# Kernel tuning notes

Hardware: AMD Instinct MI355X
Metric: run time of the kernel (lower is better)

Reference implementation:

```python
import jax, jax.numpy as jnp
import numpy as np

D_MODEL = 1024
N_HEADS = 16
D_K = D_MODEL // N_HEADS


def setup_inputs() -> dict:
    key = jax.random.key(0)
    ks = jax.random.split(key, 9)
    s = 1.0 / np.sqrt(D_MODEL)
    inp = {
        "x": jax.random.normal(ks[0], (4, 2048, D_MODEL), dtype=jnp.float32),
        "wq": jax.random.normal(ks[1], (D_MODEL, D_MODEL), dtype=jnp.float32) * s,
        "bq": jax.random.normal(ks[2], (D_MODEL,), dtype=jnp.float32) * 0.01,
        "wk": jax.random.normal(ks[3], (D_MODEL, D_MODEL), dtype=jnp.float32) * s,
        "bk": jax.random.normal(ks[4], (D_MODEL,), dtype=jnp.float32) * 0.01,
        "wv": jax.random.normal(ks[5], (D_MODEL, D_MODEL), dtype=jnp.float32) * s,
        "bv": jax.random.normal(ks[6], (D_MODEL,), dtype=jnp.float32) * 0.01,
        "wo": jax.random.normal(ks[7], (D_MODEL, D_MODEL), dtype=jnp.float32) * s,
        "bo": jax.random.normal(ks[8], (D_MODEL,), dtype=jnp.float32) * 0.01,
    }
    return inp


def reference(x, wq, bq, wk, bk, wv, bv, wo, bo):
    B, S, _ = x.shape
    # QKV projections (weights stored [in, out] so y = x @ w + b)
    q = (x @ wq + bq).reshape(B, S, N_HEADS, D_K).transpose(0, 2, 1, 3)  # [B,H,S,Dk]
    k = (x @ wk + bk).reshape(B, S, N_HEADS, D_K).transpose(0, 2, 1, 3)
    v = (x @ wv + bv).reshape(B, S, N_HEADS, D_K).transpose(0, 2, 1, 3)
    scale = 1.0 / jnp.sqrt(jnp.asarray(D_K, dtype=x.dtype))
    scores = jnp.einsum("bhqd,bhkd->bhqk", q, k) * scale  # [B,H,S,S]
    attn = jax.nn.softmax(scores, axis=-1)
    out = jnp.einsum("bhqk,bhkd->bhqd", attn, v)  # [B,H,S,Dk]
    out = out.transpose(0, 2, 1, 3).reshape(B, S, D_MODEL)
    return out @ wo + bo
```

## Files before the change

### kernel.cpp

```cpp
#include <hip/hip_runtime.h>

#define D_MODEL 1024
#define NH 16
#define DK 64
#define BB 4
#define SS 2048
#define MROWS (BB*SS)

typedef __attribute__((ext_vector_type(4))) float f32x4;
typedef __attribute__((ext_vector_type(16))) float f32x16;
typedef __attribute__((ext_vector_type(8))) short short8;
typedef __attribute__((ext_vector_type(4))) float float4v;
typedef __attribute__((ext_vector_type(2))) unsigned u32x2;

typedef const __attribute__((address_space(1))) void* gas_t;
typedef __attribute__((address_space(3))) void* las_t;

static __device__ __forceinline__ ushort f2bf(float f) {
  union { float f; unsigned u; } v; v.f = f;
  unsigned r = 0x7fffu + ((v.u >> 16) & 1u);
  return (ushort)((v.u + r) >> 16);
}

#define VM_WAIT(N)                                              \
  do {                                                          \
    asm volatile("s_waitcnt vmcnt(" #N ")" ::: "memory");       \
    __builtin_amdgcn_sched_barrier(0);                          \
  } while (0)

#define LGKM0()                                                 \
  do {                                                          \
    asm volatile("s_waitcnt lgkmcnt(0)" ::: "memory");          \
    __builtin_amdgcn_sched_barrier(0);                          \
  } while (0)

__global__ __launch_bounds__(256) void convert_x_k(const float* __restrict__ x,
                                                   ushort* __restrict__ xb) {
  int i = blockIdx.x * 256 + threadIdx.x;
  float4v v = ((const float4v*)x)[i];
  ushort4 o;
  o.x = f2bf(v.x); o.y = f2bf(v.y); o.z = f2bf(v.z); o.w = f2bf(v.w);
  ((ushort4*)xb)[i] = o;
}

__global__ __launch_bounds__(256) void convert_wt4_k(const float* __restrict__ w0,
                                                     const float* __restrict__ w1,
                                                     const float* __restrict__ w2,
                                                     const float* __restrict__ w3,
                                                     ushort* __restrict__ t0,
                                                     ushort* __restrict__ t1,
                                                     ushort* __restrict__ t2,
                                                     ushort* __restrict__ t3) {
  __shared__ float tile[64][65];
  const float* w; ushort* wt;
  switch (blockIdx.z) {
    case 0: w = w0; wt = t0; break;
    case 1: w = w1; wt = t1; break;
    case 2: w = w2; wt = t2; break;
    default: w = w3; wt = t3; break;
  }
  int bx = blockIdx.x, by = blockIdx.y;
  int tx = threadIdx.x & 63, ty = threadIdx.x >> 6;
#pragma unroll
  for (int i = 0; i < 16; ++i) {
    int r = i * 4 + ty;
    tile[r][tx] = w[(size_t)(by * 64 + r) * D_MODEL + bx * 64 + tx];
  }
  __syncthreads();
#pragma unroll
  for (int i = 0; i < 16; ++i) {
    int r = i * 4 + ty;
    wt[(size_t)(bx * 64 + r) * D_MODEL + by * 64 + tx] = f2bf(tile[tx][r]);
  }
}

__global__ __launch_bounds__(512) void gemm_qkv_k(const ushort* __restrict__ A,
                                                  const ushort* __restrict__ Bt,
                                                  const float* __restrict__ bq,
                                                  const float* __restrict__ bk,
                                                  const float* __restrict__ bv,
                                                  ushort* __restrict__ Qw,
                                                  ushort* __restrict__ Kw,
                                                  ushort* __restrict__ Vw,
                                                  float qscale) {
  const int K = D_MODEL;
  __shared__ __align__(16) ushort As[3][256 * 64];
  __shared__ __align__(16) ushort Bs[3][128 * 64];
  const int nbn = 24;
  int bid = blockIdx.x;
  int wg = (bid & 7) * 96 + (bid >> 3);
  int bm = wg / nbn, bn = wg % nbn;
  const int t = threadIdx.x;
  const int l = t & 63;
  const int w = t >> 6;
  const int g = l >> 4, q = l & 15;
  const int wr = w >> 1, wc = w & 1;
  const int qs = q & 7;

  f32x4 acc[4][4];
#pragma unroll
  for (int m = 0; m < 4; ++m)
#pragma unroll
    for (int n = 0; n < 4; ++n) acc[m][n] = f32x4{0.f, 0.f, 0.f, 0.f};

  const ushort* Ab = A + (size_t)bm * 256 * K;
  const ushort* Bb = Bt + (size_t)bn * 128 * K;

#define GSTAGE(BUF, KT)                                                                       \
  do {                                                                                        \
    _Pragma("unroll") for (int i_ = 0; i_ < 4; ++i_) {                                        \
      int c_ = i_ * 512 + t;                                                                  \
      int r_ = c_ >> 3;                                                                       \
      int gc_ = (c_ & 7) ^ (r_ & 7);                                                          \
      __builtin_amdgcn_global_load_lds((gas_t)(Ab + (size_t)r_ * K + (KT) * 64 + gc_ * 8),    \
                                       (las_t)(&As[BUF][c_ * 8]), 16, 0, 0);                  \
    }                                                                                         \
    _Pragma("unroll") for (int i_ = 0; i_ < 2; ++i_) {                                        \
      int c_ = i_ * 512 + t;                                                                  \
      int r_ = c_ >> 3;                                                                       \
      int gc_ = (c_ & 7) ^ (r_ & 7);                                                          \
      __builtin_amdgcn_global_load_lds((gas_t)(Bb + (size_t)r_ * K + (KT) * 64 + gc_ * 8),    \
                                       (las_t)(&Bs[BUF][c_ * 8]), 16, 0, 0);                  \
    }                                                                                         \
  } while (0)

  GSTAGE(0, 0);
  GSTAGE(1, 1);

  for (int kt = 0; kt < 16; ++kt) {
    if (kt + 2 < 16) {
      GSTAGE((kt + 2) % 3, kt + 2);
      VM_WAIT(12);
    } else if (kt + 1 < 16) {
      VM_WAIT(6);
    } else {
      VM_WAIT(0);
    }
    __builtin_amdgcn_s_barrier();
    __builtin_amdgcn_sched_barrier(0);

    const ushort* Ac = As[kt % 3];
    const ushort* Bc = Bs[kt % 3];

    short8 bf[4][2];
#pragma unroll
    for (int n = 0; n < 4; ++n)
#pragma unroll
      for (int ks = 0; ks < 2; ++ks)
        bf[n][ks] = *(const short8*)(Bc + (wc * 64 + n * 16 + q) * 64 + (((ks * 4 + g) ^ qs) * 8));

#pragma unroll
    for (int mh = 0; mh < 2; ++mh) {
      short8 af[2][2];
#pragma unroll
      for (int m2 = 0; m2 < 2; ++m2)
#pragma unroll
        for (int ks = 0; ks < 2; ++ks)
          af[m2][ks] = *(const short8*)(Ac + (wr * 64 + (mh * 2 + m2) * 16 + q) * 64 + (((ks * 4 + g) ^ qs) * 8));
      LGKM0();
      __builtin_amdgcn_s_setprio(1);
#pragma unroll
      for (int m2 = 0; m2 < 2; ++m2)
#pragma unroll
        for (int n = 0; n < 4; ++n)
#pragma unroll
          for (int ks = 0; ks < 2; ++ks)
            acc[mh * 2 + m2][n] =
                __builtin_amdgcn_mfma_f32_16x16x32_bf16(af[m2][ks], bf[n][ks], acc[mh * 2 + m2][n], 0, 0, 0);
      __builtin_amdgcn_s_setprio(0);
    }

    __builtin_amdgcn_sched_barrier(0);
    __builtin_amdgcn_s_barrier();
  }
#undef GSTAGE

  const int sec = (bn * 128) >> 10;
  const float* bias = sec == 0 ? bq : (sec == 1 ? bk : bv);
  const float scale = sec == 0 ? qscale : 1.0f;
  ushort* dst = sec == 0 ? Qw : Kw;
  const int rbase0 = bm * 256 + wr * 64 + g * 4;
  const int cbase = (bn * 128 + wc * 64 + q) & 1023;
#pragma unroll
  for (int m = 0; m < 4; ++m) {
    int r0 = rbase0 + m * 16;
#pragma unroll
    for (int n = 0; n < 4; ++n) {
      int c = cbase + n * 16;
      float bv_ = bias[c];
      if (sec == 2) {
        ushort4 pk;
        pk.x = f2bf(acc[m][n][0] + bv_);
        pk.y = f2bf(acc[m][n][1] + bv_);
        pk.z = f2bf(acc[m][n][2] + bv_);
        pk.w = f2bf(acc[m][n][3] + bv_);
        size_t off = (((size_t)((r0 >> 11) * NH + (c >> 6))) * DK + (c & 63)) * (size_t)SS + (r0 & (SS - 1));
        *(ushort4*)(Vw + off) = pk;
      } else {
#pragma unroll
        for (int j = 0; j < 4; ++j) {
          int r = r0 + j;
          float v = (acc[m][n][j] + bv_) * scale;
          size_t off = (((size_t)((r >> 11) * NH + (c >> 6))) * SS + (r & (SS - 1))) * DK + (c & 63);
          dst[off] = f2bf(v);
        }
      }
    }
  }
}

__global__ __launch_bounds__(256) void gemm_out_k(const ushort* __restrict__ A,
                                                  const ushort* __restrict__ Bt,
                                                  const float* __restrict__ bias,
                                                  float* __restrict__ outp) {
  const int K = D_MODEL;
  __shared__ __align__(16) ushort As[2][128 * 32];
  __shared__ __align__(16) ushort Bs[2][128 * 32];
  const int nbn = 8;
  int bid = blockIdx.x;
  int wg = (bid & 7) * 64 + (bid >> 3);
  int bm = wg / nbn, bn = wg % nbn;
  const int t = threadIdx.x;
  const int l = t & 63;
  const int w = t >> 6;
  const int g = l >> 4, q = l & 15;
  const int wr = w >> 1, wc = w & 1;

  f32x4 acc[4][4];
#pragma unroll
  for (int m = 0; m < 4; ++m)
#pragma unroll
    for (int n = 0; n < 4; ++n) acc[m][n] = f32x4{0.f, 0.f, 0.f, 0.f};

  const ushort* Ab = A + (size_t)bm * 128 * K;
  const ushort* Bb = Bt + (size_t)bn * 128 * K;

#define GSTAGE(BUF, KT)                                                                      \
  do {                                                                                       \
    _Pragma("unroll") for (int i_ = 0; i_ < 2; ++i_) {                                       \
      int c_ = i_ * 256 + t;                                                                 \
      __builtin_amdgcn_global_load_lds((gas_t)(Ab + (size_t)(c_ >> 2) * K + (KT) + (c_ & 3) * 8), \
                                       (las_t)(As[BUF] + c_ * 8), 16, 0, 0);                 \
      __builtin_amdgcn_global_load_lds((gas_t)(Bb + (size_t)(c_ >> 2) * K + (KT) + (c_ & 3) * 8), \
                                       (las_t)(Bs[BUF] + c_ * 8), 16, 0, 0);                 \
    }                                                                                        \
  } while (0)

  GSTAGE(0, 0);
  int cur = 0;

  for (int kt = 0; kt < K; kt += 32) {
    if (kt + 32 < K) {
      GSTAGE(cur ^ 1, kt + 32);
      VM_WAIT(4);
    } else {
      VM_WAIT(0);
    }
    __builtin_amdgcn_s_barrier();
    __builtin_amdgcn_sched_barrier(0);
    short8 af[4], bf[4];
#pragma unroll
    for (int m = 0; m < 4; ++m)
      af[m] = *(const short8*)(As[cur] + (wr * 64 + m * 16 + q) * 32 + g * 8);
#pragma unroll
    for (int n = 0; n < 4; ++n)
      bf[n] = *(const short8*)(Bs[cur] + (wc * 64 + n * 16 + q) * 32 + g * 8);
#pragma unroll
    for (int m = 0; m < 4; ++m)
#pragma unroll
      for (int n = 0; n < 4; ++n)
        acc[m][n] = __builtin_amdgcn_mfma_f32_16x16x32_bf16(af[m], bf[n], acc[m][n], 0, 0, 0);
    __builtin_amdgcn_sched_barrier(0);
    __builtin_amdgcn_s_barrier();
    cur ^= 1;
  }
#undef GSTAGE

  const int rbase0 = bm * 128 + wr * 64 + g * 4;
  const int cbase = bn * 128 + wc * 64 + q;
#pragma unroll
  for (int m = 0; m < 4; ++m) {
    int r0 = rbase0 + m * 16;
#pragma unroll
    for (int n = 0; n < 4; ++n) {
      int c = cbase + n * 16;
      float bv = bias[c];
#pragma unroll
      for (int j = 0; j < 4; ++j)
        outp[(size_t)(r0 + j) * D_MODEL + c] = acc[m][n][j] + bv;
    }
  }
}

__global__ __launch_bounds__(256, 4) void attn_k(const ushort* __restrict__ Qm,
                                                 const ushort* __restrict__ Km,
                                                 const ushort* __restrict__ Vm,
                                                 ushort* __restrict__ Ob) {
  __shared__ __align__(16) ushort Ks[2][64 * 64];
  __shared__ __align__(16) ushort Vs[2][64 * 64];
  const int bid = blockIdx.x;
  const int logical = (bid & 7) * 128 + (bid >> 3);
  const int bh = logical >> 4;
  const int qblk = logical & 15;
  const int t = threadIdx.x, l = t & 63, w = t >> 6;
  const int q = l & 31, h = l >> 5;
  const int qsw = q & 7;

  const ushort* Qb = Qm + ((size_t)bh * SS + qblk * 128 + w * 32) * DK;
  const ushort* Kb = Km + (size_t)bh * SS * DK;
  const ushort* Vb = Vm + (size_t)bh * DK * SS;

  short8 qf[4];
#pragma unroll
  for (int ks = 0; ks < 4; ++ks)
    qf[ks] = *(const short8*)(Qb + q * DK + ks * 16 + h * 8);

  f32x16 oacc[2];
#pragma unroll
  for (int d = 0; d < 2; ++d)
#pragma unroll
    for (int r = 0; r < 16; ++r) oacc[d][r] = 0.f;
  float lrun = 0.f;

  const int cg = (l & 7) ^ ((l >> 3) & 7);

#define STAGE(B, KT)                                                                        \
  do {                                                                                      \
    _Pragma("unroll") for (int i_ = 0; i_ < 2; ++i_) {                                      \
      int row_ = w * 16 + i_ * 8 + (l >> 3);                                                \
      __builtin_amdgcn_global_load_lds((gas_t)(Kb + (size_t)((KT) + row_) * DK + cg * 8),   \
                                       (las_t)(Ks[B] + (w * 16 + i_ * 8) * 64 + l * 8),     \
                                       16, 0, 0);                                           \
      __builtin_amdgcn_global_load_lds((gas_t)(Vb + (size_t)row_ * SS + (KT) + cg * 8),     \
                                       (las_t)(Vs[B] + (w * 16 + i_ * 8) * 64 + l * 8),     \
                                       16, 0, 0);                                           \
    }                                                                                       \
  } while (0)

  STAGE(0, 0);
  int cur = 0;

  for (int kt = 0; kt < SS; kt += 64) {
    __syncthreads();
    if (kt + 64 < SS) STAGE(cur ^ 1, kt + 64);

    const ushort* Kc = Ks[cur];
    const ushort* Vc = Vs[cur];

    f32x16 sc[2];
#pragma unroll
    for (int n = 0; n < 2; ++n)
#pragma unroll
      for (int r = 0; r < 16; ++r) sc[n][r] = 0.f;

    __builtin_amdgcn_s_setprio(1);
#pragma unroll
    for (int ks = 0; ks < 4; ++ks) {
      int ch = ((ks * 2 + h) ^ qsw) * 8;
      short8 kf0 = *(const short8*)(Kc + q * 64 + ch);
      short8 kf1 = *(const short8*)(Kc + (32 + q) * 64 + ch);
      sc[0] = __builtin_amdgcn_mfma_f32_32x32x16_bf16(kf0, qf[ks], sc[0], 0, 0, 0);
      sc[1] = __builtin_amdgcn_mfma_f32_32x32x16_bf16(kf1, qf[ks], sc[1], 0, 0, 0);
    }
    __builtin_amdgcn_s_setprio(0);

#pragma unroll
    for (int n = 0; n < 2; ++n)
#pragma unroll
      for (int r = 0; r < 16; ++r) sc[n][r] = __builtin_amdgcn_exp2f(sc[n][r]);

    float s8[8];
#pragma unroll
    for (int i = 0; i < 8; ++i)
      s8[i] = (sc[0][i] + sc[0][i + 8]) + (sc[1][i] + sc[1][i + 8]);
#pragma unroll
    for (int i = 0; i < 4; ++i) s8[i] += s8[i + 4];
    lrun += (s8[0] + s8[1]) + (s8[2] + s8[3]);

    short8 pf[4];
#pragma unroll
    for (int n = 0; n < 2; ++n) {
      unsigned wv[8];
#pragma unroll
      for (int Qd = 0; Qd < 4; ++Qd) {
        unsigned w0, w1;
        asm("v_cvt_pk_bf16_f32 %0, %1, %2" : "=v"(w0) : "v"(sc[n][Qd * 4 + 0]), "v"(sc[n][Qd * 4 + 1]));
        asm("v_cvt_pk_bf16_f32 %0, %1, %2" : "=v"(w1) : "v"(sc[n][Qd * 4 + 2]), "v"(sc[n][Qd * 4 + 3]));
        wv[Qd * 2] = w0; wv[Qd * 2 + 1] = w1;
      }
#pragma unroll
      for (int m = 0; m < 2; ++m) {
        u32x2 r0 = __builtin_amdgcn_permlane32_swap(wv[(2 * m) * 2 + 0], wv[(2 * m + 1) * 2 + 0], false, false);
        u32x2 r1 = __builtin_amdgcn_permlane32_swap(wv[(2 * m) * 2 + 1], wv[(2 * m + 1) * 2 + 1], false, false);
        union { unsigned u[4]; short8 s; } fu;
        fu.u[0] = r0[0]; fu.u[1] = r1[0]; fu.u[2] = r0[1]; fu.u[3] = r1[1];
        pf[n * 2 + m] = fu.s;
      }
    }

    __builtin_amdgcn_s_setprio(1);
#pragma unroll
    for (int kvb = 0; kvb < 4; ++kvb) {
      int ch = ((kvb * 2 + h) ^ qsw) * 8;
      short8 vf0 = *(const short8*)(Vc + q * 64 + ch);
      short8 vf1 = *(const short8*)(Vc + (32 + q) * 64 + ch);
      oacc[0] = __builtin_amdgcn_mfma_f32_32x32x16_bf16(vf0, pf[kvb], oacc[0], 0, 0, 0);
      oacc[1] = __builtin_amdgcn_mfma_f32_32x32x16_bf16(vf1, pf[kvb], oacc[1], 0, 0, 0);
    }
    __builtin_amdgcn_s_setprio(0);
    cur ^= 1;
  }
#undef STAGE

  const int b_ = bh >> 4, h_ = bh & 15;
  float lt = lrun;
  lt += __shfl_xor(lt, 32);
  float inv = 1.0f / lt;
  const int srow = qblk * 128 + w * 32 + q;
#pragma unroll
  for (int d = 0; d < 2; ++d)
#pragma unroll
    for (int rq = 0; rq < 4; ++rq) {
      ushort4 pk;
      pk.x = f2bf(oacc[d][rq * 4 + 0] * inv);
      pk.y = f2bf(oacc[d][rq * 4 + 1] * inv);
      pk.z = f2bf(oacc[d][rq * 4 + 2] * inv);
      pk.w = f2bf(oacc[d][rq * 4 + 3] * inv);
      size_t off = ((size_t)b_ * SS + srow) * D_MODEL + h_ * 64 + d * 32 + rq * 8 + h * 4;
      *(ushort4*)(Ob + off) = pk;
    }
}

extern "C" void kernel_launch(void* const* d_in, const int* in_sizes, int n_in,
                              void* d_out, int out_size, void* d_ws, size_t ws_size,
                              hipStream_t stream) {
  (void)in_sizes; (void)n_in; (void)out_size; (void)ws_size;
  const float* x  = (const float*)d_in[0];
  const float* wq = (const float*)d_in[1];
  const float* bq = (const float*)d_in[2];
  const float* wk = (const float*)d_in[3];
  const float* bk = (const float*)d_in[4];
  const float* wv = (const float*)d_in[5];
  const float* bv = (const float*)d_in[6];
  const float* wo = (const float*)d_in[7];
  const float* bo = (const float*)d_in[8];

  char* ws = (char*)d_ws;
  ushort* xb    = (ushort*)(ws);
  ushort* wqkvt = (ushort*)(ws + 16777216);
  ushort* wot   = (ushort*)(ws + 16777216 + 6291456);
  ushort* Qw    = (ushort*)(ws + 16777216 + 6291456 + 2097152);
  ushort* Kw    = (ushort*)(ws + 16777216 + 6291456 + 2097152 + 16777216);
  ushort* Vw    = (ushort*)(ws + 16777216 + 6291456 + 2097152 + 2 * 16777216);
  ushort* Obw   = xb;

  convert_x_k<<<MROWS * D_MODEL / 4 / 256, 256, 0, stream>>>(x, xb);
  convert_wt4_k<<<dim3(16, 16, 4), 256, 0, stream>>>(
      wq, wk, wv, wo, wqkvt, wqkvt + 1024 * 1024, wqkvt + 2 * 1024 * 1024, wot);

  gemm_qkv_k<<<768, 512, 0, stream>>>(xb, wqkvt, bq, bk, bv, Qw, Kw, Vw,
                                      0.125f * 1.44269504088896f);

  attn_k<<<1024, 256, 0, stream>>>(Qw, Kw, Vw, Obw);

  gemm_out_k<<<512, 256, 0, stream>>>(Obw, wot, bo, (float*)d_out);
}
```

Measured before the change: 195.7 us.

## Interleave global-to-LDS prefetch with MFMA phases and remap QKV block order

Restructures the QKV projection GEMM main loop into four k-half/m-half phases. Each phase issues part of the next-next tile's global_load_lds between its LDS fragment reads and its MFMAs, and each phase is bracketed by barriers. This aims to spread memory traffic across compute and improve overlap. Block-to-tile mapping also changes so each XCD handles a contiguous group of 4 row blocks across all column blocks, intended to improve L2 reuse of A. The extra barriers per iteration add synchronization cost.

New measurement: 197.1 us. No clear change (+0.7%).

```diff
diff --git a/kernel.cpp b/kernel.cpp
--- a/kernel.cpp
+++ b/kernel.cpp
@@ -83,13 +83,12 @@
                                                   ushort* __restrict__ Kw,
                                                   ushort* __restrict__ Vw,
                                                   float qscale) {
-  const int K = D_MODEL;
   __shared__ __align__(16) ushort As[3][256 * 64];
   __shared__ __align__(16) ushort Bs[3][128 * 64];
-  const int nbn = 24;
   int bid = blockIdx.x;
-  int wg = (bid & 7) * 96 + (bid >> 3);
-  int bm = wg / nbn, bn = wg % nbn;
+  int xcd = bid & 7, i0 = bid >> 3;
+  int bm = xcd * 4 + (i0 & 3);
+  int bn = i0 >> 2;
   const int t = threadIdx.x;
   const int l = t & 63;
   const int w = t >> 6;
@@ -103,77 +102,104 @@
 #pragma unroll
     for (int n = 0; n < 4; ++n) acc[m][n] = f32x4{0.f, 0.f, 0.f, 0.f};
 
-  const ushort* Ab = A + (size_t)bm * 256 * K;
-  const ushort* Bb = Bt + (size_t)bn * 128 * K;
-
-#define GSTAGE(BUF, KT)                                                                       \
+  const ushort* Ab = A + (size_t)bm * 256 * D_MODEL;
+  const ushort* Bb = Bt + (size_t)bn * 128 * D_MODEL;
+
+#define GL_A(BUF, KT, I)                                                                      \
   do {                                                                                        \
-    _Pragma("unroll") for (int i_ = 0; i_ < 4; ++i_) {                                        \
-      int c_ = i_ * 512 + t;                                                                  \
-      int r_ = c_ >> 3;                                                                       \
-      int gc_ = (c_ & 7) ^ (r_ & 7);                                                          \
-      __builtin_amdgcn_global_load_lds((gas_t)(Ab + (size_t)r_ * K + (KT) * 64 + gc_ * 8),    \
-                                       (las_t)(&As[BUF][c_ * 8]), 16, 0, 0);                  \
-    }                                                                                         \
-    _Pragma("unroll") for (int i_ = 0; i_ < 2; ++i_) {                                        \
-      int c_ = i_ * 512 + t;                                                                  \
-      int r_ = c_ >> 3;                                                                       \
-      int gc_ = (c_ & 7) ^ (r_ & 7);                                                          \
-      __builtin_amdgcn_global_load_lds((gas_t)(Bb + (size_t)r_ * K + (KT) * 64 + gc_ * 8),    \
-                                       (las_t)(&Bs[BUF][c_ * 8]), 16, 0, 0);                  \
-    }                                                                                         \
-  } while (0)
-
-  GSTAGE(0, 0);
-  GSTAGE(1, 1);
-
-  for (int kt = 0; kt < 16; ++kt) {
-    if (kt + 2 < 16) {
-      GSTAGE((kt + 2) % 3, kt + 2);
-      VM_WAIT(12);
-    } else if (kt + 1 < 16) {
-      VM_WAIT(6);
-    } else {
-      VM_WAIT(0);
-    }
-    __builtin_amdgcn_s_barrier();
-    __builtin_amdgcn_sched_barrier(0);
-
+    int c_ = (I) * 512 + t;                                                                   \
+    int r_ = c_ >> 3;                                                                         \
+    int gc_ = (c_ & 7) ^ (r_ & 7);                                                            \
+    __builtin_amdgcn_global_load_lds((gas_t)(Ab + (size_t)r_ * D_MODEL + (KT) * 64 + gc_ * 8),\
+                                     (las_t)(&As[BUF][c_ * 8]), 16, 0, 0);                    \
+  } while (0)
+#define GL_B(BUF, KT, I)                                                                      \
+  do {                                                                                        \
+    int c_ = (I) * 512 + t;                                                                   \
+    int r_ = c_ >> 3;                                                                         \
+    int gc_ = (c_ & 7) ^ (r_ & 7);                                                            \
+    __builtin_amdgcn_global_load_lds((gas_t)(Bb + (size_t)r_ * D_MODEL + (KT) * 64 + gc_ * 8),\
+                                     (las_t)(&Bs[BUF][c_ * 8]), 16, 0, 0);                    \
+  } while (0)
+
+  const int NT = 16;
+  GL_A(0, 0, 0); GL_A(0, 0, 1); GL_A(0, 0, 2); GL_A(0, 0, 3); GL_B(0, 0, 0); GL_B(0, 0, 1);
+  GL_A(1, 1, 0); GL_A(1, 1, 1); GL_A(1, 1, 2); GL_A(1, 1, 3); GL_B(1, 1, 0); GL_B(1, 1, 1);
+  VM_WAIT(6);
+  __builtin_amdgcn_s_barrier();
+
+  for (int kt = 0; kt < NT; ++kt) {
     const ushort* Ac = As[kt % 3];
     const ushort* Bc = Bs[kt % 3];
-
-    short8 bf[4][2];
+    const int sb = (kt + 2) % 3;
+    const int stkt = kt + 2;
+    const bool st = stkt < NT;
+    short8 bf0[4], bf1[4], af[2];
+
 #pragma unroll
     for (int n = 0; n < 4; ++n)
-#pragma unroll
-      for (int ks = 0; ks < 2; ++ks)
-        bf[n][ks] = *(const short8*)(Bc + (wc * 64 + n * 16 + q) * 64 + (((ks * 4 + g) ^ qs) * 8));
-
-#pragma unroll
-    for (int mh = 0; mh < 2; ++mh) {
-      short8 af[2][2];
-#pragma unroll
-      for (int m2 = 0; m2 < 2; ++m2)
-#pragma unroll
-        for (int ks = 0; ks < 2; ++ks)
-          af[m2][ks] = *(const short8*)(Ac + (wr * 64 + (mh * 2 + m2) * 16 + q) * 64 + (((ks * 4 + g) ^ qs) * 8));
-      LGKM0();
-      __builtin_amdgcn_s_setprio(1);
-#pragma unroll
-      for (int m2 = 0; m2 < 2; ++m2)
-#pragma unroll
-        for (int n = 0; n < 4; ++n)
-#pragma unroll
-          for (int ks = 0; ks < 2; ++ks)
-            acc[mh * 2 + m2][n] =
-                __builtin_amdgcn_mfma_f32_16x16x32_bf16(af[m2][ks], bf[n][ks], acc[mh * 2 + m2][n], 0, 0, 0);
-      __builtin_amdgcn_s_setprio(0);
-    }
-
-    __builtin_amdgcn_sched_barrier(0);
-    __builtin_amdgcn_s_barrier();
-  }
-#undef GSTAGE
+      bf0[n] = *(const short8*)(Bc + (wc * 64 + n * 16 + q) * 64 + ((g ^ qs) * 8));
+    af[0] = *(const short8*)(Ac + (wr * 64 + 0 + q) * 64 + ((g ^ qs) * 8));
+    af[1] = *(const short8*)(Ac + (wr * 64 + 16 + q) * 64 + ((g ^ qs) * 8));
+    if (st) { GL_A(sb, stkt, 0); GL_A(sb, stkt, 1); }
+    __builtin_amdgcn_s_barrier();
+    LGKM0();
+    __builtin_amdgcn_s_setprio(1);
+#pragma unroll
+    for (int m2 = 0; m2 < 2; ++m2)
+#pragma unroll
+      for (int n = 0; n < 4; ++n)
+        acc[m2][n] = __builtin_amdgcn_mfma_f32_16x16x32_bf16(af[m2], bf0[n], acc[m2][n], 0, 0, 0);
+    __builtin_amdgcn_s_setprio(0);
+    __builtin_amdgcn_s_barrier();
+
+    af[0] = *(const short8*)(Ac + (wr * 64 + 32 + q) * 64 + ((g ^ qs) * 8));
+    af[1] = *(const short8*)(Ac + (wr * 64 + 48 + q) * 64 + ((g ^ qs) * 8));
+    if (st) { GL_A(sb, stkt, 2); GL_A(sb, stkt, 3); }
+    __builtin_amdgcn_s_barrier();
+    LGKM0();
+    __builtin_amdgcn_s_setprio(1);
+#pragma unroll
+    for (int m2 = 0; m2 < 2; ++m2)
+#pragma unroll
+      for (int n = 0; n < 4; ++n)
+        acc[2 + m2][n] = __builtin_amdgcn_mfma_f32_16x16x32_bf16(af[m2], bf0[n], acc[2 + m2][n], 0, 0, 0);
+    __builtin_amdgcn_s_setprio(0);
+    __builtin_amdgcn_s_barrier();
+
+#pragma unroll
+    for (int n = 0; n < 4; ++n)
+      bf1[n] = *(const short8*)(Bc + (wc * 64 + n * 16 + q) * 64 + (((4 + g) ^ qs) * 8));
+    af[0] = *(const short8*)(Ac + (wr * 64 + 0 + q) * 64 + (((4 + g) ^ qs) * 8));
+    af[1] = *(const short8*)(Ac + (wr * 64 + 16 + q) * 64 + (((4 + g) ^ qs) * 8));
+    if (st) { GL_B(sb, stkt, 0); GL_B(sb, stkt, 1); }
+    __builtin_amdgcn_s_barrier();
+    LGKM0();
+    __builtin_amdgcn_s_setprio(1);
+#pragma unroll
+    for (int m2 = 0; m2 < 2; ++m2)
+#pragma unroll
+      for (int n = 0; n < 4; ++n)
+        acc[m2][n] = __builtin_amdgcn_mfma_f32_16x16x32_bf16(af[m2], bf1[n], acc[m2][n], 0, 0, 0);
+    __builtin_amdgcn_s_setprio(0);
+    __builtin_amdgcn_s_barrier();
+
+    af[0] = *(const short8*)(Ac + (wr * 64 + 32 + q) * 64 + (((4 + g) ^ qs) * 8));
+    af[1] = *(const short8*)(Ac + (wr * 64 + 48 + q) * 64 + (((4 + g) ^ qs) * 8));
+    __builtin_amdgcn_s_barrier();
+    LGKM0();
+    __builtin_amdgcn_s_setprio(1);
+#pragma unroll
+    for (int m2 = 0; m2 < 2; ++m2)
+#pragma unroll
+      for (int n = 0; n < 4; ++n)
+        acc[2 + m2][n] = __builtin_amdgcn_mfma_f32_16x16x32_bf16(af[m2], bf1[n], acc[2 + m2][n], 0, 0, 0);
+    __builtin_amdgcn_s_setprio(0);
+    if (kt + 2 < NT) { VM_WAIT(6); } else if (kt + 1 < NT) { VM_WAIT(0); }
+    __builtin_amdgcn_s_barrier();
+  }
+#undef GL_A
+#undef GL_B
 
   const int sec = (bn * 128) >> 10;
   const float* bias = sec == 0 ? bq : (sec == 1 ? bk : bv);
```

## Unify QKV and output GEMMs into one 256x256-tile kernel with split-stage prefetch

Applied to the files above, without the earlier changes.

Replaces the two GEMM kernels with a single templated kernel that computes 256x256 output tiles using 8 waves, each owning a 128x64 sub-tile. The main loop is double-buffered rather than triple-buffered, and the next A-tile's global-to-LDS loads are interleaved between MFMA phases. The intent is to raise arithmetic intensity and cut redundant global/LDS traffic. The cost is fewer workgroups: 384 for QKV and only 128 for the output projection, which may underfill the 256 CUs. There is also more register pressure from the 32 accumulators.

Measured after the change: 205.4 us. 5.0% more time.

```diff
diff --git a/kernel.cpp b/kernel.cpp
--- a/kernel.cpp
+++ b/kernel.cpp
@@ -74,220 +74,173 @@
   }
 }
 
-__global__ __launch_bounds__(512) void gemm_qkv_k(const ushort* __restrict__ A,
-                                                  const ushort* __restrict__ Bt,
-                                                  const float* __restrict__ bq,
-                                                  const float* __restrict__ bk,
-                                                  const float* __restrict__ bv,
-                                                  ushort* __restrict__ Qw,
-                                                  ushort* __restrict__ Kw,
-                                                  ushort* __restrict__ Vw,
-                                                  float qscale) {
-  const int K = D_MODEL;
-  __shared__ __align__(16) ushort As[3][256 * 64];
-  __shared__ __align__(16) ushort Bs[3][128 * 64];
-  const int nbn = 24;
-  int bid = blockIdx.x;
-  int wg = (bid & 7) * 96 + (bid >> 3);
-  int bm = wg / nbn, bn = wg % nbn;
+template <int MODE>
+__global__ __launch_bounds__(512) void gemm256_k(const ushort* __restrict__ A,
+                                                 const ushort* __restrict__ Bt,
+                                                 const float* __restrict__ b0,
+                                                 const float* __restrict__ b1,
+                                                 const float* __restrict__ b2,
+                                                 ushort* __restrict__ Qw,
+                                                 ushort* __restrict__ Kw,
+                                                 ushort* __restrict__ Vw,
+                                                 float* __restrict__ Fo,
+                                                 float qscale) {
+  __shared__ __align__(16) ushort AsS[2][2][8192];
+  __shared__ __align__(16) ushort BsS[2][2][8192];
+  const int bid = blockIdx.x;
+  const int xcd = bid & 7, i0 = bid >> 3;
+  const int bm = xcd * 4 + (i0 & 3);
+  const int bn = i0 >> 2;
   const int t = threadIdx.x;
   const int l = t & 63;
   const int w = t >> 6;
   const int g = l >> 4, q = l & 15;
-  const int wr = w >> 1, wc = w & 1;
+  const int wr = w >> 2;
+  const int wc = w & 3;
   const int qs = q & 7;
 
-  f32x4 acc[4][4];
-#pragma unroll
-  for (int m = 0; m < 4; ++m)
+  f32x4 acc[8][4];
+#pragma unroll
+  for (int m = 0; m < 8; ++m)
 #pragma unroll
     for (int n = 0; n < 4; ++n) acc[m][n] = f32x4{0.f, 0.f, 0.f, 0.f};
 
-  const ushort* Ab = A + (size_t)bm * 256 * K;
-  const ushort* Bb = Bt + (size_t)bn * 128 * K;
-
-#define GSTAGE(BUF, KT)                                                                       \
+  const ushort* Ab = A + (size_t)bm * 256 * D_MODEL;
+  const ushort* Bb = Bt + (size_t)bn * 256 * D_MODEL;
+
+#define STG(PS, SRC, BUFI, HF, T)                                                             \
   do {                                                                                        \
-    _Pragma("unroll") for (int i_ = 0; i_ < 4; ++i_) {                                        \
-      int c_ = i_ * 512 + t;                                                                  \
+    _Pragma("unroll") for (int s_ = 0; s_ < 2; ++s_) {                                        \
+      int c_ = s_ * 512 + t;                                                                  \
       int r_ = c_ >> 3;                                                                       \
       int gc_ = (c_ & 7) ^ (r_ & 7);                                                          \
-      __builtin_amdgcn_global_load_lds((gas_t)(Ab + (size_t)r_ * K + (KT) * 64 + gc_ * 8),    \
-                                       (las_t)(&As[BUF][c_ * 8]), 16, 0, 0);                  \
-    }                                                                                         \
-    _Pragma("unroll") for (int i_ = 0; i_ < 2; ++i_) {                                        \
-      int c_ = i_ * 512 + t;                                                                  \
-      int r_ = c_ >> 3;                                                                       \
-      int gc_ = (c_ & 7) ^ (r_ & 7);                                                          \
-      __builtin_amdgcn_global_load_lds((gas_t)(Bb + (size_t)r_ * K + (KT) * 64 + gc_ * 8),    \
-                                       (las_t)(&Bs[BUF][c_ * 8]), 16, 0, 0);                  \
+      __builtin_amdgcn_global_load_lds(                                                       \
+          (gas_t)(SRC + (size_t)((HF) * 128 + r_) * D_MODEL + (T) * 64 + gc_ * 8),            \
+          (las_t)(&PS[BUFI][HF][c_ * 8]), 16, 0, 0);                                          \
     }                                                                                         \
   } while (0)
 
-  GSTAGE(0, 0);
-  GSTAGE(1, 1);
-
-  for (int kt = 0; kt < 16; ++kt) {
-    if (kt + 2 < 16) {
-      GSTAGE((kt + 2) % 3, kt + 2);
-      VM_WAIT(12);
-    } else if (kt + 1 < 16) {
-      VM_WAIT(6);
-    } else {
-      VM_WAIT(0);
-    }
+  const int NT = 16;
+  STG(BsS, Bb, 0, 0, 0); STG(BsS, Bb, 0, 1, 0);
+  STG(AsS, Ab, 0, 0, 0); STG(AsS, Ab, 0, 1, 0);
+
+  for (int kt = 0; kt < NT; ++kt) {
+    const int buf = kt & 1, nbuf = buf ^ 1;
+    const bool st = (kt + 1) < NT;
+    const ushort* Ah = AsS[buf][wr];
+    const ushort* Bh = BsS[buf][wc >> 1];
+    const int brow = (wc & 1) * 64;
+    short8 bf[4], af[4];
+
+    if (st) { STG(BsS, Bb, nbuf, 0, kt + 1); STG(BsS, Bb, nbuf, 1, kt + 1); VM_WAIT(4); }
+    else { VM_WAIT(0); }
     __builtin_amdgcn_s_barrier();
-    __builtin_amdgcn_sched_barrier(0);
-
-    const ushort* Ac = As[kt % 3];
-    const ushort* Bc = Bs[kt % 3];
-
-    short8 bf[4][2];
 #pragma unroll
     for (int n = 0; n < 4; ++n)
-#pragma unroll
-      for (int ks = 0; ks < 2; ++ks)
-        bf[n][ks] = *(const short8*)(Bc + (wc * 64 + n * 16 + q) * 64 + (((ks * 4 + g) ^ qs) * 8));
-
-#pragma unroll
-    for (int mh = 0; mh < 2; ++mh) {
-      short8 af[2][2];
-#pragma unroll
-      for (int m2 = 0; m2 < 2; ++m2)
-#pragma unroll
-        for (int ks = 0; ks < 2; ++ks)
-          af[m2][ks] = *(const short8*)(Ac + (wr * 64 + (mh * 2 + m2) * 16 + q) * 64 + (((ks * 4 + g) ^ qs) * 8));
-      LGKM0();
-      __builtin_amdgcn_s_setprio(1);
-#pragma unroll
-      for (int m2 = 0; m2 < 2; ++m2)
-#pragma unroll
-        for (int n = 0; n < 4; ++n)
-#pragma unroll
-          for (int ks = 0; ks < 2; ++ks)
-            acc[mh * 2 + m2][n] =
-                __builtin_amdgcn_mfma_f32_16x16x32_bf16(af[m2][ks], bf[n][ks], acc[mh * 2 + m2][n], 0, 0, 0);
-      __builtin_amdgcn_s_setprio(0);
-    }
-
-    __builtin_amdgcn_sched_barrier(0);
+      bf[n] = *(const short8*)(Bh + (brow + n * 16 + q) * 64 + ((g ^ qs) * 8));
+#pragma unroll
+    for (int m2 = 0; m2 < 4; ++m2)
+      af[m2] = *(const short8*)(Ah + (m2 * 16 + q) * 64 + ((g ^ qs) * 8));
+    LGKM0();
+    __builtin_amdgcn_s_setprio(1);
+#pragma unroll
+    for (int m2 = 0; m2 < 4; ++m2)
+#pragma unroll
+      for (int n = 0; n < 4; ++n)
+        acc[m2][n] = __builtin_amdgcn_mfma_f32_16x16x32_bf16(af[m2], bf[n], acc[m2][n], 0, 0, 0);
+    __builtin_amdgcn_s_setprio(0);
     __builtin_amdgcn_s_barrier();
-  }
-#undef GSTAGE
-
-  const int sec = (bn * 128) >> 10;
-  const float* bias = sec == 0 ? bq : (sec == 1 ? bk : bv);
-  const float scale = sec == 0 ? qscale : 1.0f;
-  ushort* dst = sec == 0 ? Qw : Kw;
-  const int rbase0 = bm * 256 + wr * 64 + g * 4;
-  const int cbase = (bn * 128 + wc * 64 + q) & 1023;
-#pragma unroll
-  for (int m = 0; m < 4; ++m) {
-    int r0 = rbase0 + m * 16;
-#pragma unroll
-    for (int n = 0; n < 4; ++n) {
-      int c = cbase + n * 16;
-      float bv_ = bias[c];
-      if (sec == 2) {
-        ushort4 pk;
-        pk.x = f2bf(acc[m][n][0] + bv_);
-        pk.y = f2bf(acc[m][n][1] + bv_);
-        pk.z = f2bf(acc[m][n][2] + bv_);
-        pk.w = f2bf(acc[m][n][3] + bv_);
-        size_t off = (((size_t)((r0 >> 11) * NH + (c >> 6))) * DK + (c & 63)) * (size_t)SS + (r0 & (SS - 1));
-        *(ushort4*)(Vw + off) = pk;
-      } else {
-#pragma unroll
-        for (int j = 0; j < 4; ++j) {
-          int r = r0 + j;
-          float v = (acc[m][n][j] + bv_) * scale;
-          size_t off = (((size_t)((r >> 11) * NH + (c >> 6))) * SS + (r & (SS - 1))) * DK + (c & 63);
-          dst[off] = f2bf(v);
+
+#pragma unroll
+    for (int m2 = 0; m2 < 4; ++m2)
+      af[m2] = *(const short8*)(Ah + (64 + m2 * 16 + q) * 64 + ((g ^ qs) * 8));
+    if (st) STG(AsS, Ab, nbuf, 0, kt + 1);
+    LGKM0();
+    __builtin_amdgcn_s_setprio(1);
+#pragma unroll
+    for (int m2 = 0; m2 < 4; ++m2)
+#pragma unroll
+      for (int n = 0; n < 4; ++n)
+        acc[4 + m2][n] = __builtin_amdgcn_mfma_f32_16x16x32_bf16(af[m2], bf[n], acc[4 + m2][n], 0, 0, 0);
+    __builtin_amdgcn_s_setprio(0);
+    __builtin_amdgcn_s_barrier();
+
+#pragma unroll
+    for (int n = 0; n < 4; ++n)
+      bf[n] = *(const short8*)(Bh + (brow + n * 16 + q) * 64 + (((4 + g) ^ qs) * 8));
+#pragma unroll
+    for (int m2 = 0; m2 < 4; ++m2)
+      af[m2] = *(const short8*)(Ah + (m2 * 16 + q) * 64 + (((4 + g) ^ qs) * 8));
+    if (st) STG(AsS, Ab, nbuf, 1, kt + 1);
+    LGKM0();
+    __builtin_amdgcn_s_setprio(1);
+#pragma unroll
+    for (int m2 = 0; m2 < 4; ++m2)
+#pragma unroll
+      for (int n = 0; n < 4; ++n)
+        acc[m2][n] = __builtin_amdgcn_mfma_f32_16x16x32_bf16(af[m2], bf[n], acc[m2][n], 0, 0, 0);
+    __builtin_amdgcn_s_setprio(0);
+    __builtin_amdgcn_s_barrier();
+
+#pragma unroll
+    for (int m2 = 0; m2 < 4; ++m2)
+      af[m2] = *(const short8*)(Ah + (64 + m2 * 16 + q) * 64 + (((4 + g) ^ qs) * 8));
+    LGKM0();
+    __builtin_amdgcn_s_setprio(1);
+#pragma unroll
+    for (int m2 = 0; m2 < 4; ++m2)
+#pragma unroll
+      for (int n = 0; n < 4; ++n)
+        acc[4 + m2][n] = __builtin_amdgcn_mfma_f32_16x16x32_bf16(af[m2], bf[n], acc[4 + m2][n], 0, 0, 0);
+    __builtin_amdgcn_s_setprio(0);
+    __builtin_amdgcn_s_barrier();
+  }
+#undef STG
+
+  if (MODE == 1) {
+#pragma unroll
+    for (int mf = 0; mf < 8; ++mf) {
+      int r0 = bm * 256 + wr * 128 + mf * 16 + g * 4;
+#pragma unroll
+      for (int nf = 0; nf < 4; ++nf) {
+        int c = bn * 256 + wc * 64 + nf * 16 + q;
+        float bv = b0[c];
+#pragma unroll
+        for (int j = 0; j < 4; ++j)
+          Fo[(size_t)(r0 + j) * D_MODEL + c] = acc[mf][nf][j] + bv;
+      }
+    }
+  } else {
+    const int sec = (bn * 256) >> 10;
+    const float* bias = sec == 0 ? b0 : (sec == 1 ? b1 : b2);
+    const float scale = sec == 0 ? qscale : 1.0f;
+    ushort* dst = sec == 0 ? Qw : Kw;
+#pragma unroll
+    for (int mf = 0; mf < 8; ++mf) {
+      int r0 = bm * 256 + wr * 128 + mf * 16 + g * 4;
+#pragma unroll
+      for (int nf = 0; nf < 4; ++nf) {
+        int cg_ = bn * 256 + wc * 64 + nf * 16 + q;
+        int c = cg_ & 1023;
+        float bv_ = bias[c];
+        if (sec == 2) {
+          ushort4 pk;
+          pk.x = f2bf(acc[mf][nf][0] + bv_);
+          pk.y = f2bf(acc[mf][nf][1] + bv_);
+          pk.z = f2bf(acc[mf][nf][2] + bv_);
+          pk.w = f2bf(acc[mf][nf][3] + bv_);
+          size_t off = (((size_t)((r0 >> 11) * NH + (c >> 6))) * DK + (c & 63)) * (size_t)SS + (r0 & (SS - 1));
+          *(ushort4*)(Vw + off) = pk;
+        } else {
+#pragma unroll
+          for (int j = 0; j < 4; ++j) {
+            int r = r0 + j;
+            float v = (acc[mf][nf][j] + bv_) * scale;
+            size_t off = (((size_t)((r >> 11) * NH + (c >> 6))) * SS + (r & (SS - 1))) * DK + (c & 63);
+            dst[off] = f2bf(v);
+          }
         }
       }
-    }
-  }
-}
-
-__global__ __launch_bounds__(256) void gemm_out_k(const ushort* __restrict__ A,
-                                                  const ushort* __restrict__ Bt,
-                                                  const float* __restrict__ bias,
-                                                  float* __restrict__ outp) {
-  const int K = D_MODEL;
-  __shared__ __align__(16) ushort As[2][128 * 32];
-  __shared__ __align__(16) ushort Bs[2][128 * 32];
-  const int nbn = 8;
-  int bid = blockIdx.x;
-  int wg = (bid & 7) * 64 + (bid >> 3);
-  int bm = wg / nbn, bn = wg % nbn;
-  const int t = threadIdx.x;
-  const int l = t & 63;
-  const int w = t >> 6;
-  const int g = l >> 4, q = l & 15;
-  const int wr = w >> 1, wc = w & 1;
-
-  f32x4 acc[4][4];
-#pragma unroll
-  for (int m = 0; m < 4; ++m)
-#pragma unroll
-    for (int n = 0; n < 4; ++n) acc[m][n] = f32x4{0.f, 0.f, 0.f, 0.f};
-
-  const ushort* Ab = A + (size_t)bm * 128 * K;
-  const ushort* Bb = Bt + (size_t)bn * 128 * K;
-
-#define GSTAGE(BUF, KT)                                                                      \
-  do {                                                                                       \
-    _Pragma("unroll") for (int i_ = 0; i_ < 2; ++i_) {                                       \
-      int c_ = i_ * 256 + t;                                                                 \
-      __builtin_amdgcn_global_load_lds((gas_t)(Ab + (size_t)(c_ >> 2) * K + (KT) + (c_ & 3) * 8), \
-                                       (las_t)(As[BUF] + c_ * 8), 16, 0, 0);                 \
-      __builtin_amdgcn_global_load_lds((gas_t)(Bb + (size_t)(c_ >> 2) * K + (KT) + (c_ & 3) * 8), \
-                                       (las_t)(Bs[BUF] + c_ * 8), 16, 0, 0);                 \
-    }                                                                                        \
-  } while (0)
-
-  GSTAGE(0, 0);
-  int cur = 0;
-
-  for (int kt = 0; kt < K; kt += 32) {
-    if (kt + 32 < K) {
-      GSTAGE(cur ^ 1, kt + 32);
-      VM_WAIT(4);
-    } else {
-      VM_WAIT(0);
-    }
-    __builtin_amdgcn_s_barrier();
-    __builtin_amdgcn_sched_barrier(0);
-    short8 af[4], bf[4];
-#pragma unroll
-    for (int m = 0; m < 4; ++m)
-      af[m] = *(const short8*)(As[cur] + (wr * 64 + m * 16 + q) * 32 + g * 8);
-#pragma unroll
-    for (int n = 0; n < 4; ++n)
-      bf[n] = *(const short8*)(Bs[cur] + (wc * 64 + n * 16 + q) * 32 + g * 8);
-#pragma unroll
-    for (int m = 0; m < 4; ++m)
-#pragma unroll
-      for (int n = 0; n < 4; ++n)
-        acc[m][n] = __builtin_amdgcn_mfma_f32_16x16x32_bf16(af[m], bf[n], acc[m][n], 0, 0, 0);
-    __builtin_amdgcn_sched_barrier(0);
-    __builtin_amdgcn_s_barrier();
-    cur ^= 1;
-  }
-#undef GSTAGE
-
-  const int rbase0 = bm * 128 + wr * 64 + g * 4;
-  const int cbase = bn * 128 + wc * 64 + q;
-#pragma unroll
-  for (int m = 0; m < 4; ++m) {
-    int r0 = rbase0 + m * 16;
-#pragma unroll
-    for (int n = 0; n < 4; ++n) {
-      int c = cbase + n * 16;
-      float bv = bias[c];
-#pragma unroll
-      for (int j = 0; j < 4; ++j)
-        outp[(size_t)(r0 + j) * D_MODEL + c] = acc[m][n][j] + bv;
     }
   }
 }
@@ -458,10 +411,11 @@
   convert_wt4_k<<<dim3(16, 16, 4), 256, 0, stream>>>(
       wq, wk, wv, wo, wqkvt, wqkvt + 1024 * 1024, wqkvt + 2 * 1024 * 1024, wot);
 
-  gemm_qkv_k<<<768, 512, 0, stream>>>(xb, wqkvt, bq, bk, bv, Qw, Kw, Vw,
-                                      0.125f * 1.44269504088896f);
+  gemm256_k<0><<<384, 512, 0, stream>>>(xb, wqkvt, bq, bk, bv, Qw, Kw, Vw, nullptr,
+                                        0.125f * 1.44269504088896f);
 
   attn_k<<<1024, 256, 0, stream>>>(Qw, Kw, Vw, Obw);
 
-  gemm_out_k<<<512, 256, 0, stream>>>(Obw, wot, bo, (float*)d_out);
-}
+  gemm256_k<1><<<128, 512, 0, stream>>>(Obw, wot, bo, nullptr, nullptr,
+                                        nullptr, nullptr, nullptr, (float*)d_out, 1.0f);
+}
```
